# Performance work log

Measured on AMD Instinct MI355X. Metric: run time of the kernel, lower is better.

The kernel has to match this reference:

```python
import jax, jax.numpy as jnp
import numpy as np

N_NODES = 50000
N_EDGES = 800000
D_IN = 128
D_HID = 256
D_OUT = 256


def setup_inputs() -> dict:
    key = jax.random.key(0)
    ks = jax.random.split(key, 16)
    x = jax.random.normal(ks[0], (N_NODES, D_IN), dtype=jnp.float32)
    src = jax.random.randint(ks[1], (N_EDGES,), 0, N_NODES)
    dst = jax.random.randint(ks[2], (N_EDGES,), 0, N_NODES)

    def w(k, fan_in, fan_out):
        return jax.random.normal(k, (fan_in, fan_out), dtype=jnp.float32) / np.sqrt(fan_in)

    return {
        "x": x, "src": src, "dst": dst,
        "Ws0": w(ks[3], D_IN, D_HID), "Wn0": w(ks[4], D_IN, D_HID), "b0": jnp.zeros((D_HID,), jnp.float32),
        "Ws1": w(ks[5], D_HID, D_HID), "Wn1": w(ks[6], D_HID, D_HID), "b1": jnp.zeros((D_HID,), jnp.float32),
        "Ws2": w(ks[7], D_HID, D_OUT), "Wn2": w(ks[8], D_HID, D_OUT), "b2": jnp.zeros((D_OUT,), jnp.float32),
    }


def _sage_layer(h, src, dst, Ws, Wn, b, n_nodes):
    # mean aggregation: gather src features per edge, segment-sum into dst, divide by in-degree
    msg_sum = jax.ops.segment_sum(h[src], dst, num_segments=n_nodes)          # [N, d]
    deg = jax.ops.segment_sum(jnp.ones((src.shape[0],), h.dtype), dst, num_segments=n_nodes)
    h_neigh = msg_sum / jnp.maximum(deg, 1.0)[:, None]                        # zero in-degree -> 0
    return jax.nn.relu(h @ Ws + h_neigh @ Wn + b)


def reference(x, src, dst, Ws0, Wn0, b0, Ws1, Wn1, b1, Ws2, Wn2, b2):
    n = x.shape[0]
    h = _sage_layer(x, src, dst, Ws0, Wn0, b0, n)
    h = _sage_layer(h, src, dst, Ws1, Wn1, b1, n)
    h = _sage_layer(h, src, dst, Ws2, Wn2, b2, n)
    return h
```

## Files before the change

### kernel.cpp

```cpp
#include <hip/hip_runtime.h>
#include <hip/hip_bf16.h>

#define NN 50000
#define NE 800000

typedef __attribute__((ext_vector_type(8))) _Float16 half8v;
typedef __attribute__((ext_vector_type(4))) _Float16 half4v;
typedef __attribute__((ext_vector_type(2))) _Float16 half2v;
typedef __attribute__((ext_vector_type(4))) float f32x4;

__device__ __forceinline__ void gload_lds16(const void* g, void* l) {
  __builtin_amdgcn_global_load_lds((const __attribute__((address_space(1))) void*)g,
                                   (__attribute__((address_space(3))) void*)l, 16, 0, 0);
}
__device__ __forceinline__ void vm_wait5() {
  asm volatile("s_waitcnt vmcnt(5)" ::: "memory");
  __builtin_amdgcn_sched_barrier(0);
}
__device__ __forceinline__ void vm_wait0() {
  asm volatile("s_waitcnt vmcnt(0)" ::: "memory");
  __builtin_amdgcn_sched_barrier(0);
}
__device__ __forceinline__ void barx() {
  __builtin_amdgcn_sched_barrier(0);
  __builtin_amdgcn_s_barrier();
  __builtin_amdgcn_sched_barrier(0);
}

__global__ void k_zero(int* __restrict__ p, int n) {
  int i = blockIdx.x * blockDim.x + threadIdx.x;
  if (i < n) p[i] = 0;
}

__global__ void k_count(const int* __restrict__ dst, int* __restrict__ cnt) {
  int i = blockIdx.x * blockDim.x + threadIdx.x;
  int st = gridDim.x * blockDim.x;
  for (; i < NE; i += st) atomicAdd(&cnt[dst[i]], 1);
}

__global__ __launch_bounds__(1024) void k_scan(int* __restrict__ cnt, int* __restrict__ rowptr) {
  __shared__ int wsum[16];
  __shared__ int woff[16];
  __shared__ int tot;
  const int tid = threadIdx.x;
  const int lane = tid & 63;
  const int w = tid >> 6;
  int running = 0;
  for (int base = 0; base < NN; base += 1024) {
    int i = base + tid;
    int v = (i < NN) ? cnt[i] : 0;
    int x = v;
#pragma unroll
    for (int off = 1; off < 64; off <<= 1) {
      int t = __shfl_up(x, off);
      if (lane >= off) x += t;
    }
    if (lane == 63) wsum[w] = x;
    __syncthreads();
    if (w == 0) {
      int s = (lane < 16) ? wsum[lane] : 0;
#pragma unroll
      for (int off = 1; off < 16; off <<= 1) {
        int t = __shfl_up(s, off);
        if (lane >= off) s += t;
      }
      if (lane < 16) woff[lane] = s - wsum[lane];
      if (lane == 15) tot = s;
    }
    __syncthreads();
    if (i < NN) {
      int excl = running + woff[w] + (x - v);
      rowptr[i] = excl;
      cnt[i] = excl;
    }
    running += tot;
    __syncthreads();
  }
  if (tid == 0) rowptr[NN] = running;
}

__global__ void k_fill(const int* __restrict__ src, const int* __restrict__ dst,
                       int* __restrict__ cursor, int* __restrict__ col) {
  int i = blockIdx.x * blockDim.x + threadIdx.x;
  int st = gridDim.x * blockDim.x;
  for (; i < NE; i += st) {
    int p = atomicAdd(&cursor[dst[i]], 1);
    col[p] = src[i];
  }
}

__global__ void k_wpack(const float* __restrict__ W, _Float16* __restrict__ Wp, int K) {
  int t = blockIdx.x * blockDim.x + threadIdx.x;
  if (t >= K * 32) return;
  int l = t & 63;
  int c = (t >> 6) & 15;
  int kb = t >> 10;
  int row = c * 16 + (l & 15);
  int k = kb * 32 + (l >> 4) * 8;
  half8v o;
#pragma unroll
  for (int i = 0; i < 8; ++i) o[i] = (_Float16)W[(size_t)(k + i) * 256 + row];
  *reinterpret_cast<half8v*>(Wp + (size_t)t * 8) = o;
}

__global__ void k_split16(const float* __restrict__ x, _Float16* __restrict__ X16) {
  int t = blockIdx.x * blockDim.x + threadIdx.x;
  if (t >= NN * 16) return;
  const float* p = x + (size_t)t * 8;
  float4 v0 = *reinterpret_cast<const float4*>(p);
  float4 v1 = *reinterpret_cast<const float4*>(p + 4);
  half8v o;
  o[0] = (_Float16)v0.x; o[1] = (_Float16)v0.y; o[2] = (_Float16)v0.z; o[3] = (_Float16)v0.w;
  o[4] = (_Float16)v1.x; o[5] = (_Float16)v1.y; o[6] = (_Float16)v1.z; o[7] = (_Float16)v1.w;
  *reinterpret_cast<half8v*>(X16 + (size_t)t * 8) = o;
}

__global__ __launch_bounds__(256) void k_agg_x16(const float* __restrict__ x,
                                                 const int* __restrict__ rowptr,
                                                 const int* __restrict__ col,
                                                 _Float16* __restrict__ N) {
  const int lane = threadIdx.x & 63;
  const int n = blockIdx.x * 4 + (threadIdx.x >> 6);
  if (n >= NN) return;
  const int start = rowptr[n];
  const int end = rowptr[n + 1];
  float a0 = 0.f, a1 = 0.f;
  for (int base = start; base < end; base += 64) {
    int e = base + lane;
    int c = (e < end) ? col[e] : 0;
    int m = min(64, end - base);
    int t = 0;
    for (; t + 3 < m; t += 4) {
      int c0 = __shfl(c, t), c1 = __shfl(c, t + 1), c2 = __shfl(c, t + 2), c3 = __shfl(c, t + 3);
      float2 v0 = *reinterpret_cast<const float2*>(x + (size_t)c0 * 128 + lane * 2);
      float2 v1 = *reinterpret_cast<const float2*>(x + (size_t)c1 * 128 + lane * 2);
      float2 v2 = *reinterpret_cast<const float2*>(x + (size_t)c2 * 128 + lane * 2);
      float2 v3 = *reinterpret_cast<const float2*>(x + (size_t)c3 * 128 + lane * 2);
      a0 += v0.x + v1.x + v2.x + v3.x;
      a1 += v0.y + v1.y + v2.y + v3.y;
    }
    for (; t < m; ++t) {
      int cs = __shfl(c, t);
      float2 v = *reinterpret_cast<const float2*>(x + (size_t)cs * 128 + lane * 2);
      a0 += v.x;
      a1 += v.y;
    }
  }
  int deg = end - start;
  float sc = 1.0f / (float)(deg > 0 ? deg : 1);
  half2v o;
  o[0] = (_Float16)(a0 * sc);
  o[1] = (_Float16)(a1 * sc);
  *reinterpret_cast<half2v*>(N + (size_t)n * 128 + lane * 2) = o;
}

__global__ __launch_bounds__(256) void k_agg16(const _Float16* __restrict__ H,
                                               const int* __restrict__ rowptr,
                                               const int* __restrict__ col,
                                               _Float16* __restrict__ N) {
  const int lane = threadIdx.x & 63;
  const int n = blockIdx.x * 4 + (threadIdx.x >> 6);
  if (n >= NN) return;
  const int start = rowptr[n];
  const int end = rowptr[n + 1];
  float a0 = 0.f, a1 = 0.f, a2 = 0.f, a3 = 0.f;
  for (int base = start; base < end; base += 64) {
    int e = base + lane;
    int c = (e < end) ? col[e] : 0;
    int m = min(64, end - base);
    int t = 0;
    for (; t + 3 < m; t += 4) {
      int c0 = __shfl(c, t), c1 = __shfl(c, t + 1), c2 = __shfl(c, t + 2), c3 = __shfl(c, t + 3);
      half4v v0 = *reinterpret_cast<const half4v*>(H + (size_t)c0 * 256 + lane * 4);
      half4v v1 = *reinterpret_cast<const half4v*>(H + (size_t)c1 * 256 + lane * 4);
      half4v v2 = *reinterpret_cast<const half4v*>(H + (size_t)c2 * 256 + lane * 4);
      half4v v3 = *reinterpret_cast<const half4v*>(H + (size_t)c3 * 256 + lane * 4);
      a0 += (float)v0[0] + (float)v1[0] + (float)v2[0] + (float)v3[0];
      a1 += (float)v0[1] + (float)v1[1] + (float)v2[1] + (float)v3[1];
      a2 += (float)v0[2] + (float)v1[2] + (float)v2[2] + (float)v3[2];
      a3 += (float)v0[3] + (float)v1[3] + (float)v2[3] + (float)v3[3];
    }
    for (; t < m; ++t) {
      int cs = __shfl(c, t);
      half4v v = *reinterpret_cast<const half4v*>(H + (size_t)cs * 256 + lane * 4);
      a0 += (float)v[0];
      a1 += (float)v[1];
      a2 += (float)v[2];
      a3 += (float)v[3];
    }
  }
  int deg = end - start;
  float sc = 1.0f / (float)(deg > 0 ? deg : 1);
  half4v o;
  o[0] = (_Float16)(a0 * sc);
  o[1] = (_Float16)(a1 * sc);
  o[2] = (_Float16)(a2 * sc);
  o[3] = (_Float16)(a3 * sc);
  *reinterpret_cast<half4v*>(N + (size_t)n * 256 + lane * 4) = o;
}

__global__ __launch_bounds__(256) void k_mfma16(
    const _Float16* __restrict__ A1, const _Float16* __restrict__ A2,
    const _Float16* __restrict__ W1p, const _Float16* __restrict__ W2p,
    const float* __restrict__ bias, int K,
    _Float16* __restrict__ outH, float* __restrict__ outF) {
  __shared__ _Float16 LDS[20480];
  const int tid = threadIdx.x;
  const int w = tid >> 6;
  const int lane = tid & 63;
  const int lrow = lane & 15;
  const int kg8 = (lane >> 4) * 8;
  const int m0 = blockIdx.x * 64;
  const int nk = K >> 5;
  const int nsteps = nk * 2;

  f32x4 acc[4][4];
#pragma unroll
  for (int i = 0; i < 4; ++i)
#pragma unroll
    for (int j = 0; j < 4; ++j) acc[i][j] = (f32x4){0.f, 0.f, 0.f, 0.f};

  int arowi = m0 + w * 16 + lrow;
  const size_t arow = (size_t)(arowi < NN ? arowi : NN - 1);

#define STAGE(S, B)                                                            \
  {                                                                            \
    const _Float16* Ap = ((S) >= nk) ? A2 : A1;                                \
    const _Float16* Wp = ((S) >= nk) ? W2p : W1p;                              \
    const int sl = ((S) >= nk) ? (S) - nk : (S);                               \
    gload_lds16(Ap + arow * K + (sl << 5) + kg8,                               \
                (void*)&LDS[(B) * 10240 + w * 512]);                           \
    const _Float16* wsrc = Wp + (size_t)(sl * 16 + w * 4) * 512 + lane * 8;    \
    _Pragma("unroll") for (int j = 0; j < 4; ++j)                              \
        gload_lds16(wsrc + j * 512,                                            \
                    (void*)&LDS[(B) * 10240 + 2048 + (w * 4 + j) * 512]);      \
  }

#define COMPUTE(B)                                                             \
  {                                                                            \
    half8v af[4];                                                              \
    _Pragma("unroll") for (int rf = 0; rf < 4; ++rf)                           \
        af[rf] = *reinterpret_cast<const half8v*>(                             \
            &LDS[(B) * 10240 + rf * 512 + lane * 8]);                          \
    _Pragma("unroll") for (int cf = 0; cf < 4; ++cf) {                         \
      half8v bf = *reinterpret_cast<const half8v*>(                            \
          &LDS[(B) * 10240 + 2048 + (w * 4 + cf) * 512 + lane * 8]);           \
      _Pragma("unroll") for (int rf = 0; rf < 4; ++rf)                         \
          acc[rf][cf] = __builtin_amdgcn_mfma_f32_16x16x32_f16(                \
              af[rf], bf, acc[rf][cf], 0, 0, 0);                               \
    }                                                                          \
  }

  STAGE(0, 0);
  STAGE(1, 1);
  vm_wait5();
  barx();
  for (int s = 0; s < nsteps; ++s) {
    COMPUTE(s & 1);
    barx();
    if (s + 2 < nsteps) {
      STAGE(s + 2, s & 1);
      vm_wait5();
    } else {
      vm_wait0();
    }
    barx();
  }
#undef STAGE
#undef COMPUTE

  const int rquad = (lane >> 4) * 4;
  if (outF) {
#pragma unroll
    for (int cf = 0; cf < 4; ++cf) {
      const int colc = w * 64 + cf * 16 + lrow;
      const float bb = bias[colc];
#pragma unroll
      for (int rf = 0; rf < 4; ++rf)
#pragma unroll
        for (int j = 0; j < 4; ++j) {
          const int row = m0 + rf * 16 + rquad + j;
          if (row < NN) {
            float v = acc[rf][cf][j] + bb;
            outF[(size_t)row * 256 + colc] = v > 0.f ? v : 0.f;
          }
        }
    }
  } else {
#pragma unroll
    for (int cf = 0; cf < 4; ++cf) {
      const int colc = w * 64 + cf * 16 + lrow;
      const float bb = bias[colc];
#pragma unroll
      for (int rf = 0; rf < 4; ++rf)
#pragma unroll
        for (int j = 0; j < 4; ++j) {
          float v = acc[rf][cf][j] + bb;
          LDS[(rf * 16 + rquad + j) * 264 + colc] = (_Float16)(v > 0.f ? v : 0.f);
        }
    }
    __syncthreads();
    const int row = tid >> 2;
    const int q = tid & 3;
    if (m0 + row < NN) {
#pragma unroll
      for (int it = 0; it < 8; ++it)
        *reinterpret_cast<half8v*>(outH + (size_t)(m0 + row) * 256 + q * 64 + it * 8) =
            *reinterpret_cast<const half8v*>(&LDS[row * 264 + q * 64 + it * 8]);
    }
  }
}

extern "C" void kernel_launch(void* const* d_in, const int* in_sizes, int n_in,
                              void* d_out, int out_size, void* d_ws, size_t ws_size,
                              hipStream_t stream) {
  const float* x   = (const float*)d_in[0];
  const int* src   = (const int*)d_in[1];
  const int* dst   = (const int*)d_in[2];
  const float* Ws0 = (const float*)d_in[3];
  const float* Wn0 = (const float*)d_in[4];
  const float* b0  = (const float*)d_in[5];
  const float* Ws1 = (const float*)d_in[6];
  const float* Wn1 = (const float*)d_in[7];
  const float* b1  = (const float*)d_in[8];
  const float* Ws2 = (const float*)d_in[9];
  const float* Wn2 = (const float*)d_in[10];
  const float* b2  = (const float*)d_in[11];
  float* out = (float*)d_out;

  char* ws = (char*)d_ws;
  size_t off = 0;
  auto alloc = [&](size_t bytes) {
    void* p = ws + off;
    off = (off + bytes + 255) & ~(size_t)255;
    return p;
  };
  _Float16* X16 = (_Float16*)alloc((size_t)NN * 128 * 2);
  _Float16* H   = (_Float16*)alloc((size_t)NN * 256 * 2);
  _Float16* Nb  = (_Float16*)alloc((size_t)NN * 256 * 2);
  int* rowptr = (int*)alloc((size_t)(NN + 1) * sizeof(int));
  int* cnt    = (int*)alloc((size_t)NN * sizeof(int));
  int* col    = (int*)alloc((size_t)NE * sizeof(int));
  _Float16* W0s = (_Float16*)alloc(256 * 128 * 2);
  _Float16* W0n = (_Float16*)alloc(256 * 128 * 2);
  _Float16* W1s = (_Float16*)alloc(256 * 256 * 2);
  _Float16* W1n = (_Float16*)alloc(256 * 256 * 2);
  _Float16* W2s = (_Float16*)alloc(256 * 256 * 2);
  _Float16* W2n = (_Float16*)alloc(256 * 256 * 2);

  k_zero<<<(NN + 1023) / 1024, 1024, 0, stream>>>(cnt, NN);
  k_count<<<1024, 256, 0, stream>>>(dst, cnt);
  k_scan<<<1, 1024, 0, stream>>>(cnt, rowptr);
  k_fill<<<1024, 256, 0, stream>>>(src, dst, cnt, col);

  k_wpack<<<16, 256, 0, stream>>>(Ws0, W0s, 128);
  k_wpack<<<16, 256, 0, stream>>>(Wn0, W0n, 128);
  k_wpack<<<32, 256, 0, stream>>>(Ws1, W1s, 256);
  k_wpack<<<32, 256, 0, stream>>>(Wn1, W1n, 256);
  k_wpack<<<32, 256, 0, stream>>>(Ws2, W2s, 256);
  k_wpack<<<32, 256, 0, stream>>>(Wn2, W2n, 256);

  k_split16<<<(NN * 16 + 255) / 256, 256, 0, stream>>>(x, X16);

  const int aggGrid = (NN + 3) / 4;
  const int gemmGrid = (NN + 63) / 64;

  k_agg_x16<<<aggGrid, 256, 0, stream>>>(x, rowptr, col, Nb);
  k_mfma16<<<gemmGrid, 256, 0, stream>>>(X16, Nb, W0s, W0n, b0, 128, H, nullptr);
  k_agg16<<<aggGrid, 256, 0, stream>>>(H, rowptr, col, Nb);
  k_mfma16<<<gemmGrid, 256, 0, stream>>>(H, Nb, W1s, W1n, b1, 256, H, nullptr);
  k_agg16<<<aggGrid, 256, 0, stream>>>(H, rowptr, col, Nb);
  k_mfma16<<<gemmGrid, 256, 0, stream>>>(H, Nb, W2s, W2n, b2, 256, nullptr, out);
}
```

Before: 505.7 us.

## Build CSR via two-level bucket radix pass instead of global scattered atomics

Replaces the per-edge global atomic count and fill with a first pass that bins edges into 64-node buckets, packing the source and the low destination bits into one word. Per-bucket kernels then count with LDS atomics and fill the column array with localized atomics. Edges beyond a bucket's fixed capacity go to a small overflow list. The scan is also vectorized to int4. The aim is to cut contention and scattered memory traffic during CSR construction. The risk is that edges are silently dropped if the overflow list fills up, and the overflow encoding assumes source indices fit in 16 bits.

```diff
diff --git a/kernel.cpp b/kernel.cpp
--- a/kernel.cpp
+++ b/kernel.cpp
@@ -3,6 +3,9 @@
 
 #define NN 50000
 #define NE 800000
+#define NB 782
+#define BCAP 1536
+#define OVFCAP 4096
 
 typedef __attribute__((ext_vector_type(8))) _Float16 half8v;
 typedef __attribute__((ext_vector_type(4))) _Float16 half4v;
@@ -32,10 +35,46 @@
   if (i < n) p[i] = 0;
 }
 
-__global__ void k_count(const int* __restrict__ dst, int* __restrict__ cnt) {
-  int i = blockIdx.x * blockDim.x + threadIdx.x;
-  int st = gridDim.x * blockDim.x;
-  for (; i < NE; i += st) atomicAdd(&cnt[dst[i]], 1);
+__global__ void k_radix(const int* __restrict__ src, const int* __restrict__ dst,
+                        int* __restrict__ bcur, uint* __restrict__ pairs,
+                        int* __restrict__ cnt, int* __restrict__ ovfn,
+                        uint* __restrict__ ovf) {
+  int t = blockIdx.x * blockDim.x + threadIdx.x;
+  if (t * 4 >= NE) return;
+  int4 s4 = reinterpret_cast<const int4*>(src)[t];
+  int4 d4 = reinterpret_cast<const int4*>(dst)[t];
+  int ss[4] = {s4.x, s4.y, s4.z, s4.w};
+  int dd[4] = {d4.x, d4.y, d4.z, d4.w};
+#pragma unroll
+  for (int j = 0; j < 4; ++j) {
+    int b = dd[j] >> 6;
+    int p = atomicAdd(&bcur[b], 1);
+    if (p < BCAP) {
+      pairs[(size_t)b * BCAP + p] = ((uint)ss[j] << 6) | (uint)(dd[j] & 63);
+    } else {
+      int oi = atomicAdd(ovfn, 1);
+      if (oi < OVFCAP) ovf[oi] = ((uint)dd[j] << 16) | (uint)ss[j];
+      atomicAdd(&cnt[dd[j]], 1);
+    }
+  }
+}
+
+__global__ __launch_bounds__(256) void k_countb(const int* __restrict__ bcur,
+                                                const uint* __restrict__ pairs,
+                                                int* __restrict__ cnt) {
+  __shared__ int lc[64];
+  const int b = blockIdx.x;
+  if (threadIdx.x < 64) lc[threadIdx.x] = 0;
+  __syncthreads();
+  const int m = min(bcur[b], BCAP);
+  for (int e = threadIdx.x; e < m; e += 256)
+    atomicAdd(&lc[pairs[(size_t)b * BCAP + e] & 63], 1);
+  __syncthreads();
+  if (threadIdx.x < 64) {
+    int node = b * 64 + threadIdx.x;
+    int v = lc[threadIdx.x];
+    if (node < NN && v) atomicAdd(&cnt[node], v);
+  }
 }
 
 __global__ __launch_bounds__(1024) void k_scan(int* __restrict__ cnt, int* __restrict__ rowptr) {
@@ -46,10 +85,12 @@
   const int lane = tid & 63;
   const int w = tid >> 6;
   int running = 0;
-  for (int base = 0; base < NN; base += 1024) {
-    int i = base + tid;
-    int v = (i < NN) ? cnt[i] : 0;
-    int x = v;
+  for (int base = 0; base < NN; base += 4096) {
+    const int i4 = (base >> 2) + tid;
+    int4 v = make_int4(0, 0, 0, 0);
+    if (i4 * 4 < NN) v = reinterpret_cast<const int4*>(cnt)[i4];
+    const int tsum = v.x + v.y + v.z + v.w;
+    int x = tsum;
 #pragma unroll
     for (int off = 1; off < 64; off <<= 1) {
       int t = __shfl_up(x, off);
@@ -68,10 +109,15 @@
       if (lane == 15) tot = s;
     }
     __syncthreads();
-    if (i < NN) {
-      int excl = running + woff[w] + (x - v);
-      rowptr[i] = excl;
-      cnt[i] = excl;
+    if (i4 * 4 < NN) {
+      int excl = running + woff[w] + (x - tsum);
+      int4 r;
+      r.x = excl;
+      r.y = excl + v.x;
+      r.z = r.y + v.y;
+      r.w = r.z + v.z;
+      reinterpret_cast<int4*>(rowptr)[i4] = r;
+      reinterpret_cast<int4*>(cnt)[i4] = r;
     }
     running += tot;
     __syncthreads();
@@ -79,13 +125,27 @@
   if (tid == 0) rowptr[NN] = running;
 }
 
-__global__ void k_fill(const int* __restrict__ src, const int* __restrict__ dst,
-                       int* __restrict__ cursor, int* __restrict__ col) {
-  int i = blockIdx.x * blockDim.x + threadIdx.x;
-  int st = gridDim.x * blockDim.x;
-  for (; i < NE; i += st) {
-    int p = atomicAdd(&cursor[dst[i]], 1);
-    col[p] = src[i];
+__global__ __launch_bounds__(256) void k_fillb(const int* __restrict__ bcur,
+                                               const uint* __restrict__ pairs,
+                                               int* __restrict__ cursor,
+                                               int* __restrict__ col) {
+  const int b = blockIdx.x;
+  const int m = min(bcur[b], BCAP);
+  for (int e = threadIdx.x; e < m; e += 256) {
+    uint u = pairs[(size_t)b * BCAP + e];
+    int node = b * 64 + (int)(u & 63);
+    int p = atomicAdd(&cursor[node], 1);
+    col[p] = (int)(u >> 6);
+  }
+}
+
+__global__ void k_fillovf(const int* __restrict__ ovfn, const uint* __restrict__ ovf,
+                          int* __restrict__ cursor, int* __restrict__ col) {
+  int n = min(*ovfn, OVFCAP);
+  for (int i = threadIdx.x; i < n; i += 256) {
+    uint u = ovf[i];
+    int p = atomicAdd(&cursor[u >> 16], 1);
+    col[p] = (int)(u & 0xFFFFu);
   }
 }
 
@@ -339,8 +399,14 @@
   _Float16* H   = (_Float16*)alloc((size_t)NN * 256 * 2);
   _Float16* Nb  = (_Float16*)alloc((size_t)NN * 256 * 2);
   int* rowptr = (int*)alloc((size_t)(NN + 1) * sizeof(int));
-  int* cnt    = (int*)alloc((size_t)NN * sizeof(int));
+  const int ZN = 50048 + 1024 + 64;
+  int* meta = (int*)alloc((size_t)ZN * sizeof(int));
+  int* cnt  = meta;
+  int* bcur = meta + 50048;
+  int* ovfn = meta + 50048 + 1024;
   int* col    = (int*)alloc((size_t)NE * sizeof(int));
+  uint* pairs = (uint*)alloc((size_t)NB * BCAP * sizeof(uint));
+  uint* ovf   = (uint*)alloc((size_t)OVFCAP * sizeof(uint));
   _Float16* W0s = (_Float16*)alloc(256 * 128 * 2);
   _Float16* W0n = (_Float16*)alloc(256 * 128 * 2);
   _Float16* W1s = (_Float16*)alloc(256 * 256 * 2);
@@ -348,10 +414,12 @@
   _Float16* W2s = (_Float16*)alloc(256 * 256 * 2);
   _Float16* W2n = (_Float16*)alloc(256 * 256 * 2);
 
-  k_zero<<<(NN + 1023) / 1024, 1024, 0, stream>>>(cnt, NN);
-  k_count<<<1024, 256, 0, stream>>>(dst, cnt);
+  k_zero<<<(ZN + 1023) / 1024, 1024, 0, stream>>>(meta, ZN);
+  k_radix<<<(NE / 4 + 255) / 256, 256, 0, stream>>>(src, dst, bcur, pairs, cnt, ovfn, ovf);
+  k_countb<<<NB, 256, 0, stream>>>(bcur, pairs, cnt);
   k_scan<<<1, 1024, 0, stream>>>(cnt, rowptr);
-  k_fill<<<1024, 256, 0, stream>>>(src, dst, cnt, col);
+  k_fillb<<<NB, 256, 0, stream>>>(bcur, pairs, cnt, col);
+  k_fillovf<<<1, 256, 0, stream>>>(ovfn, ovf, cnt, col);
 
   k_wpack<<<16, 256, 0, stream>>>(Ws0, W0s, 128);
   k_wpack<<<16, 256, 0, stream>>>(Wn0, W0n, 128);
```

Result: slower. 608.8 us (+20.4%).
